# Performance work log

Hardware: AMD Instinct MI355X
Metric: run time of the kernel (lower is better)

Reference implementation:

```python
import jax, jax.numpy as jnp
import numpy as np

B = 16384

def setup_inputs() -> dict:
    key = jax.random.key(0)
    k1, k2, k3 = jax.random.split(key, 3)
    predictions = jax.random.uniform(k1, (B, 7 * 7 * 30), dtype=jnp.float32)
    targets = jax.random.uniform(k2, (B, 7 * 7 * 25), dtype=jnp.float32)
    # channel 4 of each grid cell is the object-present indicator, compared to exactly 1
    t = targets.reshape(B, 7, 7, 25)
    present = (jax.random.uniform(k3, (B, 7, 7)) > 0.5).astype(jnp.float32)
    t = t.at[..., 4].set(present)
    targets = t.reshape(B, 7 * 7 * 25)
    return {"predictions": predictions, "targets": targets}


def reference(predictions, targets):
    num_batches = predictions.shape[0]
    p = predictions.reshape(num_batches, 7, 7, 30)
    t = targets.reshape(num_batches, 7, 7, 25)

    c1 = p[..., 4]
    c2 = p[..., 9]
    c = t[..., 4]
    present = (c == 1.0)
    responsible1 = c1 > c2  # box 1 is responsible

    # objectiveness loss
    obj_present = jnp.where(responsible1, jnp.square(c1 - c), jnp.square(c2 - c))
    obj_absent = 0.5 * (jnp.square(c1) + jnp.square(c2))
    obj_loss = jnp.sum(jnp.where(present, obj_present, obj_absent))

    # classification loss (only where object present)
    cls_sq = jnp.sum(jnp.square(p[..., 10:30] - t[..., 5:25]), axis=-1)  # [B,7,7]
    class_loss = jnp.sum(jnp.where(present, cls_sq, 0.0))

    r = responsible1[..., None]
    p_center = jnp.where(r, p[..., 0:2], p[..., 5:7])
    p_hw = jnp.where(r, p[..., 2:4], p[..., 7:9])
    t_center = t[..., 0:2]
    t_hw = t[..., 2:4]
    box_sq = (jnp.sum(jnp.square(p_center - t_center), axis=-1)
              + jnp.sum(jnp.square(jnp.sqrt(p_hw) - jnp.sqrt(t_hw)), axis=-1))  # [B,7,7]
    box_loss = 5.0 * jnp.sum(jnp.where(present, box_sq, 0.0))

    return obj_loss + class_loss + box_loss
```

## Files before the change

### kernel.cpp

```cpp
#include <hip/hip_runtime.h>


#define TPB 128
#define PRED_CH 30
#define TARG_CH 25
#define PRED_PAD 31

__global__ __launch_bounds__(TPB) void yolo_loss_kernel(
    const float* __restrict__ pred,
    const float* __restrict__ targ,
    float* __restrict__ out)
{
    __shared__ float sp[TPB * PRED_PAD];
    __shared__ float st[TPB * TARG_CH];

    const int tid   = threadIdx.x;
    const int cell0 = blockIdx.x * TPB;

    {
        const float4* gp = reinterpret_cast<const float4*>(pred + (size_t)cell0 * PRED_CH);
        for (int i = tid; i < (TPB * PRED_CH) / 4; i += TPB) {
            float4 v = gp[i];
            int f = i * 4;
            #pragma unroll
            for (int j = 0; j < 4; ++j) {
                int ff = f + j;
                int c  = ff / PRED_CH;
                int ch = ff - c * PRED_CH;
                sp[c * PRED_PAD + ch] = (&v.x)[j];
            }
        }
    }
    {
        const float4* gt = reinterpret_cast<const float4*>(targ + (size_t)cell0 * TARG_CH);
        float4* st4 = reinterpret_cast<float4*>(st);
        for (int i = tid; i < (TPB * TARG_CH) / 4; i += TPB)
            st4[i] = gt[i];
    }
    __syncthreads();

    const float* pv = sp + tid * PRED_PAD;
    const float* tv = st + tid * TARG_CH;

    float c1 = pv[4], c2 = pv[9], cc = tv[4];
    bool present = (cc == 1.0f);
    bool resp1   = (c1 > c2);

    float d1 = c1 - cc, d2 = c2 - cc;
    float obj_present = resp1 ? d1 * d1 : d2 * d2;
    float obj_absent  = 0.5f * (c1 * c1 + c2 * c2);
    float obj = present ? obj_present : obj_absent;

    float cls = 0.0f;
    #pragma unroll
    for (int k = 0; k < 20; ++k) {
        float d = pv[10 + k] - tv[5 + k];
        cls += d * d;
    }

    float pc0 = resp1 ? pv[0] : pv[5];
    float pc1 = resp1 ? pv[1] : pv[6];
    float ph0 = resp1 ? pv[2] : pv[7];
    float ph1 = resp1 ? pv[3] : pv[8];
    float b0 = pc0 - tv[0];
    float b1 = pc1 - tv[1];
    float s0 = sqrtf(ph0) - sqrtf(tv[2]);
    float s1 = sqrtf(ph1) - sqrtf(tv[3]);
    float box = b0 * b0 + b1 * b1 + s0 * s0 + s1 * s1;

    float loss = obj + (present ? (cls + 5.0f * box) : 0.0f);

    #pragma unroll
    for (int off = 32; off > 0; off >>= 1)
        loss += __shfl_down(loss, off);

    __shared__ float warp_sums[TPB / 64];
    int wid  = tid >> 6;
    int lane = tid & 63;
    if (lane == 0) warp_sums[wid] = loss;
    __syncthreads();

    if (tid == 0) {
        float s = warp_sums[0] + warp_sums[1];
        atomicAdd(out, s);
    }
}

extern "C" void kernel_launch(void* const* d_in, const int* in_sizes, int n_in,
                              void* d_out, int out_size, void* d_ws, size_t ws_size,
                              hipStream_t stream)
{
    const float* pred = (const float*)d_in[0];
    const float* targ = (const float*)d_in[1];
    float* out = (float*)d_out;

    hipMemsetAsync(out, 0, sizeof(float), stream);

    int ncells = in_sizes[0] / PRED_CH;
    int blocks = ncells / TPB;
    hipLaunchKernelGGL(yolo_loss_kernel, dim3(blocks), dim3(TPB), 0, stream,
                       pred, targ, out);
}
```

Baseline: 240.6 us.

## Use direct global-to-LDS loads with persistent blocks looping over tiles

Replaces the register-staged float4 copy into shared memory with the global_load_lds builtin, so data goes straight from global memory into LDS. The grid is cut to a fixed 1568 blocks, each handling four tiles of 128 cells. This reduces the number of atomics and block launch overhead. The pad that avoided bank conflicts is removed and the sizes are hardcoded to the test batch, which risks LDS bank conflicts on the stride-30 and stride-25 reads and breaks for other input sizes.

```diff
diff --git a/kernel.cpp b/kernel.cpp
--- a/kernel.cpp
+++ b/kernel.cpp
@@ -1,89 +1,101 @@
 #include <hip/hip_runtime.h>
+#include <stdint.h>
 
 
-#define TPB 128
-#define PRED_CH 30
-#define TARG_CH 25
-#define PRED_PAD 31
+#define TPB    128
+#define CELLS  128
+#define NTILES 6272
+#define GRID   1568
+#define KTILES 4
+#define P_F4   960
+#define T_F4   800
+
+#define GL2LDS(gptr, lptr)                                                    \
+    __builtin_amdgcn_global_load_lds(                                         \
+        (const __attribute__((address_space(1))) void*)(gptr),                \
+        (__attribute__((address_space(3))) void*)(uintptr_t)(lptr), 16, 0, 0)
 
 __global__ __launch_bounds__(TPB) void yolo_loss_kernel(
     const float* __restrict__ pred,
     const float* __restrict__ targ,
     float* __restrict__ out)
 {
-    __shared__ float sp[TPB * PRED_PAD];
-    __shared__ float st[TPB * TARG_CH];
+    __shared__ float4 sp4[P_F4];
+    __shared__ float4 st4[T_F4];
 
-    const int tid   = threadIdx.x;
-    const int cell0 = blockIdx.x * TPB;
+    const int tid = threadIdx.x;
+    const float* sp = (const float*)sp4;
+    const float* st = (const float*)st4;
 
-    {
-        const float4* gp = reinterpret_cast<const float4*>(pred + (size_t)cell0 * PRED_CH);
-        for (int i = tid; i < (TPB * PRED_CH) / 4; i += TPB) {
-            float4 v = gp[i];
-            int f = i * 4;
-            #pragma unroll
-            for (int j = 0; j < 4; ++j) {
-                int ff = f + j;
-                int c  = ff / PRED_CH;
-                int ch = ff - c * PRED_CH;
-                sp[c * PRED_PAD + ch] = (&v.x)[j];
-            }
+    float loss = 0.0f;
+    int tile = blockIdx.x;
+
+    for (int j = 0; j < KTILES; ++j) {
+        const float4* gp = (const float4*)pred + (size_t)tile * P_F4;
+        const float4* gt = (const float4*)targ + (size_t)tile * T_F4;
+        #pragma unroll
+        for (int r = 0; r < 7; ++r) GL2LDS(gp + tid + r * TPB, sp4 + tid + r * TPB);
+        if (tid < 64)               GL2LDS(gp + 896 + tid,     sp4 + 896 + tid);
+        #pragma unroll
+        for (int r = 0; r < 6; ++r) GL2LDS(gt + tid + r * TPB, st4 + tid + r * TPB);
+        if (tid < 32)               GL2LDS(gt + 768 + tid,     st4 + 768 + tid);
+
+        __syncthreads();
+
+        const float2* pv2 = (const float2*)(sp + tid * 30);
+        float pv[30];
+        #pragma unroll
+        for (int i = 0; i < 15; ++i) {
+            float2 v = pv2[i];
+            pv[2*i] = v.x; pv[2*i+1] = v.y;
         }
+        const float* tvp = st + tid * 25;
+        float tv[25];
+        #pragma unroll
+        for (int i = 0; i < 25; ++i) tv[i] = tvp[i];
+
+        float c1 = pv[4], c2 = pv[9], cc = tv[4];
+        bool present = (cc == 1.0f);
+        bool resp1   = (c1 > c2);
+
+        float d1 = c1 - cc, d2 = c2 - cc;
+        float obj_present = resp1 ? d1 * d1 : d2 * d2;
+        float obj_absent  = 0.5f * (c1 * c1 + c2 * c2);
+        float obj = present ? obj_present : obj_absent;
+
+        float cls = 0.0f;
+        #pragma unroll
+        for (int k = 0; k < 20; ++k) {
+            float d = pv[10 + k] - tv[5 + k];
+            cls += d * d;
+        }
+
+        float pc0 = resp1 ? pv[0] : pv[5];
+        float pc1 = resp1 ? pv[1] : pv[6];
+        float ph0 = resp1 ? pv[2] : pv[7];
+        float ph1 = resp1 ? pv[3] : pv[8];
+        float b0 = pc0 - tv[0];
+        float b1 = pc1 - tv[1];
+        float s0 = sqrtf(ph0) - sqrtf(tv[2]);
+        float s1 = sqrtf(ph1) - sqrtf(tv[3]);
+        float box = b0 * b0 + b1 * b1 + s0 * s0 + s1 * s1;
+
+        loss += obj + (present ? (cls + 5.0f * box) : 0.0f);
+
+        __syncthreads();
+        tile += GRID;
     }
-    {
-        const float4* gt = reinterpret_cast<const float4*>(targ + (size_t)cell0 * TARG_CH);
-        float4* st4 = reinterpret_cast<float4*>(st);
-        for (int i = tid; i < (TPB * TARG_CH) / 4; i += TPB)
-            st4[i] = gt[i];
-    }
-    __syncthreads();
-
-    const float* pv = sp + tid * PRED_PAD;
-    const float* tv = st + tid * TARG_CH;
-
-    float c1 = pv[4], c2 = pv[9], cc = tv[4];
-    bool present = (cc == 1.0f);
-    bool resp1   = (c1 > c2);
-
-    float d1 = c1 - cc, d2 = c2 - cc;
-    float obj_present = resp1 ? d1 * d1 : d2 * d2;
-    float obj_absent  = 0.5f * (c1 * c1 + c2 * c2);
-    float obj = present ? obj_present : obj_absent;
-
-    float cls = 0.0f;
-    #pragma unroll
-    for (int k = 0; k < 20; ++k) {
-        float d = pv[10 + k] - tv[5 + k];
-        cls += d * d;
-    }
-
-    float pc0 = resp1 ? pv[0] : pv[5];
-    float pc1 = resp1 ? pv[1] : pv[6];
-    float ph0 = resp1 ? pv[2] : pv[7];
-    float ph1 = resp1 ? pv[3] : pv[8];
-    float b0 = pc0 - tv[0];
-    float b1 = pc1 - tv[1];
-    float s0 = sqrtf(ph0) - sqrtf(tv[2]);
-    float s1 = sqrtf(ph1) - sqrtf(tv[3]);
-    float box = b0 * b0 + b1 * b1 + s0 * s0 + s1 * s1;
-
-    float loss = obj + (present ? (cls + 5.0f * box) : 0.0f);
 
     #pragma unroll
     for (int off = 32; off > 0; off >>= 1)
         loss += __shfl_down(loss, off);
 
     __shared__ float warp_sums[TPB / 64];
-    int wid  = tid >> 6;
-    int lane = tid & 63;
-    if (lane == 0) warp_sums[wid] = loss;
+    if ((tid & 63) == 0) warp_sums[tid >> 6] = loss;
     __syncthreads();
 
-    if (tid == 0) {
-        float s = warp_sums[0] + warp_sums[1];
-        atomicAdd(out, s);
-    }
+    if (tid == 0)
+        atomicAdd(out, warp_sums[0] + warp_sums[1]);
 }
 
 extern "C" void kernel_launch(void* const* d_in, const int* in_sizes, int n_in,
@@ -96,8 +108,6 @@
 
     hipMemsetAsync(out, 0, sizeof(float), stream);
 
-    int ncells = in_sizes[0] / PRED_CH;
-    int blocks = ncells / TPB;
-    hipLaunchKernelGGL(yolo_loss_kernel, dim3(blocks), dim3(TPB), 0, stream,
+    hipLaunchKernelGGL(yolo_loss_kernel, dim3(GRID), dim3(TPB), 0, stream,
                        pred, targ, out);
 }
```

Result: faster. 197.9 us (-17.8%).
